# Performance work log

Measured on AMD Instinct MI355X. Metric: run time of the kernel, lower is better.

The kernel has to match this reference:

```python
import jax, jax.numpy as jnp
import numpy as np

N = 20000
E = 320000
F_IN = 256
HID = 32
HEADS = 8
EDGE_DIM = HID // 4  # 8
NEG_SLOPE = 0.2


def _gat_conv(x, src, dst, e_emb, W, att_s, att_d, W_e, att_e, bias, H, C):
    """PyG-style GATConv with edge_dim, add_self_loops=True (fill_value='mean'), concat heads."""
    n = x.shape[0]
    loop = jnp.arange(n, dtype=src.dtype)
    # self-loop edge_attr = scatter-mean of edge_attr by dst (0 for isolated nodes)
    deg = jax.ops.segment_sum(jnp.ones_like(dst, dtype=x.dtype), dst, num_segments=n)
    e_mean = jax.ops.segment_sum(e_emb, dst, num_segments=n) / jnp.maximum(deg, 1.0)[:, None]
    src_a = jnp.concatenate([src, loop])
    dst_a = jnp.concatenate([dst, loop])
    e_all = jnp.concatenate([e_emb, e_mean], axis=0)  # [E+N, edge_dim]

    h = (x @ W).reshape(n, H, C)                      # [N,H,C]
    a_src = jnp.einsum('nhc,hc->nh', h, att_s)        # [N,H]
    a_dst = jnp.einsum('nhc,hc->nh', h, att_d)
    he = (e_all @ W_e).reshape(-1, H, C)              # [E+N,H,C]
    a_edge = jnp.einsum('ehc,hc->eh', he, att_e)      # [E+N,H]

    alpha = jax.nn.leaky_relu(a_src[src_a] + a_dst[dst_a] + a_edge, NEG_SLOPE)
    # segment softmax over destination nodes
    amax = jax.ops.segment_max(alpha, dst_a, num_segments=n)
    alpha = jnp.exp(alpha - amax[dst_a])
    denom = jax.ops.segment_sum(alpha, dst_a, num_segments=n)
    alpha = alpha / (denom[dst_a] + 1e-16)

    msg = h[src_a] * alpha[:, :, None]                # [E+N,H,C]
    out = jax.ops.segment_sum(msg, dst_a, num_segments=n)  # [N,H,C]
    return out.reshape(n, H * C) + bias


def setup_inputs() -> dict:
    key = jax.random.key(0)
    ks = jax.random.split(key, 16)

    def glorot(k, shape):
        fan_in, fan_out = shape[0], shape[-1]
        s = np.sqrt(6.0 / (fan_in + fan_out))
        return jax.random.uniform(k, shape, jnp.float32, -s, s)

    x = jax.random.normal(ks[0], (N, F_IN), jnp.float32)
    edge_index = jax.random.randint(ks[1], (2, E), 0, N, jnp.int32)
    edge_attr = jax.random.uniform(ks[2], (E, 2), jnp.float32)

    # spatial_embed: Linear(2 -> EDGE_DIM)
    Wse = glorot(ks[3], (2, EDGE_DIM))
    bse = jnp.zeros((EDGE_DIM,), jnp.float32)
    # conv1: in=F_IN, heads=HEADS, out=HID, edge_dim=EDGE_DIM
    W1 = glorot(ks[4], (F_IN, HEADS * HID))
    as1 = glorot(ks[5], (HEADS, HID))
    ad1 = glorot(ks[6], (HEADS, HID))
    We1 = glorot(ks[7], (EDGE_DIM, HEADS * HID))
    ae1 = glorot(ks[8], (HEADS, HID))
    b1 = jnp.zeros((HEADS * HID,), jnp.float32)
    # conv2: in=HEADS*HID, heads=1, out=HID
    W2 = glorot(ks[9], (HEADS * HID, HID))
    as2 = glorot(ks[10], (1, HID))
    ad2 = glorot(ks[11], (1, HID))
    We2 = glorot(ks[12], (EDGE_DIM, HID))
    ae2 = glorot(ks[13], (1, HID))
    b2 = jnp.zeros((HID,), jnp.float32)

    return {"x": x, "edge_index": edge_index, "edge_attr": edge_attr,
            "Wse": Wse, "bse": bse,
            "W1": W1, "as1": as1, "ad1": ad1, "We1": We1, "ae1": ae1, "b1": b1,
            "W2": W2, "as2": as2, "ad2": ad2, "We2": We2, "ae2": ae2, "b2": b2}


def reference(x, edge_index, edge_attr, Wse, bse,
              W1, as1, ad1, We1, ae1, b1,
              W2, as2, ad2, We2, ae2, b2):
    src, dst = edge_index[0], edge_index[1]
    e = jax.nn.relu(edge_attr @ Wse + bse)            # [E, EDGE_DIM]
    h = _gat_conv(x, src, dst, e, W1, as1, ad1, We1, ae1, b1, HEADS, HID)
    h = jax.nn.relu(h)                                # dropout inactive (eval)
    out = _gat_conv(h, src, dst, e, W2, as2, ad2, We2, ae2, b2, 1, HID)
    return out
```

## Files before the change

kernel.cpp:

```cpp
#include <hip/hip_runtime.h>
#include <hip/hip_bf16.h>
#include <float.h>


typedef short v8s __attribute__((ext_vector_type(8)));
typedef float v4f __attribute__((ext_vector_type(4)));

__device__ __forceinline__ ushort f2bf(float f) {
  unsigned u = __float_as_uint(f);
  u = (u + 0x7FFF + ((u >> 16) & 1)) >> 16;
  return (ushort)u;
}
__device__ __forceinline__ float bf2f(ushort h) {
  return __uint_as_float(((unsigned)h) << 16);
}
__device__ __forceinline__ unsigned pk2bf(float lo, float hi) {
  return (unsigned)f2bf(lo) | ((unsigned)f2bf(hi) << 16);
}

__global__ __launch_bounds__(256) void k_pre(const int* __restrict__ dst,
                                             const float* __restrict__ W1,
                                             const float* __restrict__ We1,
                                             const float* __restrict__ ae1,
                                             const float* __restrict__ We2,
                                             const float* __restrict__ ae2,
                                             int* __restrict__ deg,
                                             ushort* __restrict__ Bt,
                                             float* __restrict__ M1,
                                             float* __restrict__ m2,
                                             int E, int DB) {
  int b = blockIdx.x;
  if (b < DB) {
    int e = b * 256 + threadIdx.x;
    if (e < E) atomicAdd(&deg[dst[e]], 1);
    return;
  }
  if (b == DB + 64) {
    int t = threadIdx.x;
    if (t < 64) {
      int k = t >> 3, h = t & 7;
      float s = 0.f;
      for (int c = 0; c < 32; c++) s += We1[k * 256 + h * 32 + c] * ae1[h * 32 + c];
      M1[k * 8 + h] = s;
    } else if (t < 72) {
      int k = t - 64;
      float s = 0.f;
      for (int c = 0; c < 32; c++) s += We2[k * 32 + c] * ae2[c];
      m2[k] = s;
    }
    return;
  }
  int b2 = b - DB;
  __shared__ float tile[32][33];
  int bx = b2 & 7, by = b2 >> 3;
  int tx = threadIdx.x & 31, ty = threadIdx.x >> 5;
  for (int r = ty; r < 32; r += 8)
    tile[r][tx] = W1[(size_t)(by * 32 + r) * 256 + bx * 32 + tx];
  __syncthreads();
  for (int r = ty; r < 32; r += 8)
    Bt[(size_t)(bx * 32 + r) * 256 + by * 32 + tx] = f2bf(tile[tx][r]);
}

__global__ __launch_bounds__(1024) void k_scan(const int* __restrict__ deg,
                                               int* __restrict__ row_ptr, int N) {
  __shared__ int part[1024];
  int tid = threadIdx.x;
  int chunk = (N + 1023) / 1024;
  int lo = tid * chunk;
  if (lo > N) lo = N;
  int hi = lo + chunk;
  if (hi > N) hi = N;
  int s = 0;
  for (int i = lo; i < hi; i++) s += deg[i];
  part[tid] = s;
  __syncthreads();
  for (int off = 1; off < 1024; off <<= 1) {
    int v = 0;
    if (tid >= off) v = part[tid - off];
    __syncthreads();
    part[tid] += v;
    __syncthreads();
  }
  int base = part[tid] - s;
  for (int i = lo; i < hi; i++) { row_ptr[i] = base; base += deg[i]; }
  if (tid == 1023) row_ptr[N] = part[1023];
}

__global__ void k_scatter(const int* __restrict__ src, const int* __restrict__ dst,
                          const float* __restrict__ ea,
                          const float* __restrict__ Wse, const float* __restrict__ bse,
                          const float* __restrict__ M1, const float* __restrict__ m2,
                          const int* __restrict__ row_ptr, int* __restrict__ cursor,
                          int* __restrict__ csr_src, float* __restrict__ csr_aed1,
                          float* __restrict__ csr_aed2, int E) {
  __shared__ float sW[16], sb[8], sM[64], sm2[8];
  int t = threadIdx.x;
  if (t < 16) sW[t] = Wse[t];
  if (t < 8) sb[t] = bse[t];
  if (t < 64) sM[t] = M1[t];
  if (t >= 64 && t < 72) sm2[t - 64] = m2[t - 64];
  __syncthreads();
  int i = blockIdx.x * blockDim.x + t;
  if (i >= E) return;
  float2 av = ((const float2*)ea)[i];
  float e8[8];
#pragma unroll
  for (int k = 0; k < 8; k++)
    e8[k] = fmaxf(av.x * sW[k] + av.y * sW[8 + k] + sb[k], 0.f);
  float o[8];
#pragma unroll
  for (int h = 0; h < 8; h++) {
    float s = 0.f;
#pragma unroll
    for (int k = 0; k < 8; k++) s += e8[k] * sM[k * 8 + h];
    o[h] = s;
  }
  float s2 = 0.f;
#pragma unroll
  for (int k = 0; k < 8; k++) s2 += e8[k] * sm2[k];
  int d = dst[i];
  int pos = row_ptr[d] + atomicAdd(&cursor[d], 1);
  csr_src[pos] = src[i];
  *(float4*)(csr_aed1 + (size_t)pos * 8)     = make_float4(o[0], o[1], o[2], o[3]);
  *(float4*)(csr_aed1 + (size_t)pos * 8 + 4) = make_float4(o[4], o[5], o[6], o[7]);
  csr_aed2[pos] = s2;
}

__global__ __launch_bounds__(256) void k_gemm1_mfma(const float* __restrict__ A,
                                                    const ushort* __restrict__ Bt,
                                                    const float* __restrict__ as1,
                                                    const float* __restrict__ ad1,
                                                    ushort* __restrict__ h1b,
                                                    float* __restrict__ asv,
                                                    float* __restrict__ adv, int M) {
  __shared__ ushort sA[64 * 40];
  __shared__ ushort sB[256 * 40];
  __shared__ float sas[256], sad[256];
  int t = threadIdx.x;
  int wave = t >> 6, lane = t & 63;
  int m0 = blockIdx.x * 64;
  int c = lane & 15, kg = lane >> 4;
  sas[t] = as1[t];
  sad[t] = ad1[t];
  v4f acc[4][4];
#pragma unroll
  for (int a = 0; a < 4; a++)
#pragma unroll
    for (int b = 0; b < 4; b++) acc[a][b] = (v4f)(0.f);
  int arow = t >> 2;
  int akoff = (t & 3) * 8;
  bool aval = (m0 + arow) < M;
  const float* aptr = A + (size_t)(m0 + arow) * 256 + akoff;
  const ushort* bptr = Bt + (size_t)t * 256;
  for (int k0 = 0; k0 < 256; k0 += 32) {
    float4 v0 = make_float4(0.f, 0.f, 0.f, 0.f), v1 = v0;
    if (aval) { v0 = *(const float4*)(aptr + k0); v1 = *(const float4*)(aptr + k0 + 4); }
    unsigned* dst32 = (unsigned*)&sA[arow * 40 + akoff];
    dst32[0] = pk2bf(v0.x, v0.y);
    dst32[1] = pk2bf(v0.z, v0.w);
    dst32[2] = pk2bf(v1.x, v1.y);
    dst32[3] = pk2bf(v1.z, v1.w);
    *(v8s*)&sB[t * 40 + 0]  = *(const v8s*)(bptr + k0 + 0);
    *(v8s*)&sB[t * 40 + 8]  = *(const v8s*)(bptr + k0 + 8);
    *(v8s*)&sB[t * 40 + 16] = *(const v8s*)(bptr + k0 + 16);
    *(v8s*)&sB[t * 40 + 24] = *(const v8s*)(bptr + k0 + 24);
    __syncthreads();
    v8s af[4], bfr[4];
#pragma unroll
    for (int mt = 0; mt < 4; mt++) af[mt] = *(v8s*)&sA[(mt * 16 + c) * 40 + kg * 8];
#pragma unroll
    for (int nt = 0; nt < 4; nt++) bfr[nt] = *(v8s*)&sB[(wave * 64 + nt * 16 + c) * 40 + kg * 8];
#pragma unroll
    for (int mt = 0; mt < 4; mt++)
#pragma unroll
      for (int nt = 0; nt < 4; nt++)
        acc[mt][nt] = __builtin_amdgcn_mfma_f32_16x16x32_bf16(af[mt], bfr[nt], acc[mt][nt], 0, 0, 0);
    __syncthreads();
  }
  int colbase = wave * 64;
#pragma unroll
  for (int mt = 0; mt < 4; mt++) {
#pragma unroll
    for (int i = 0; i < 4; i++) {
      int m = m0 + mt * 16 + kg * 4 + i;
      if (m < M) {
#pragma unroll
        for (int nt = 0; nt < 4; nt++)
          h1b[(size_t)m * 256 + colbase + nt * 16 + c] = f2bf(acc[mt][nt][i]);
      }
      float s1a = acc[mt][0][i] * sas[colbase + c]      + acc[mt][1][i] * sas[colbase + 16 + c];
      float s2a = acc[mt][0][i] * sad[colbase + c]      + acc[mt][1][i] * sad[colbase + 16 + c];
      float s1b = acc[mt][2][i] * sas[colbase + 32 + c] + acc[mt][3][i] * sas[colbase + 48 + c];
      float s2b = acc[mt][2][i] * sad[colbase + 32 + c] + acc[mt][3][i] * sad[colbase + 48 + c];
#pragma unroll
      for (int o = 1; o < 16; o <<= 1) {
        s1a += __shfl_xor(s1a, o);
        s2a += __shfl_xor(s2a, o);
        s1b += __shfl_xor(s1b, o);
        s2b += __shfl_xor(s2b, o);
      }
      if (c == 0 && m < M) {
        asv[(size_t)m * 8 + 2 * wave]     = s1a;
        adv[(size_t)m * 8 + 2 * wave]     = s2a;
        asv[(size_t)m * 8 + 2 * wave + 1] = s1b;
        adv[(size_t)m * 8 + 2 * wave + 1] = s2b;
      }
    }
  }
}

__global__ __launch_bounds__(64) void k_conv1(
    const int* __restrict__ row_ptr, const int* __restrict__ csr_src,
    const float* __restrict__ csr_aed1, const float* __restrict__ asv,
    const float* __restrict__ adv, const ushort* __restrict__ h1b,
    const float* __restrict__ b1, ushort* __restrict__ h2b, int N) {
  int n = blockIdx.x;
  int lane = threadIdx.x;
  int h = lane >> 3;
  int sub = lane & 7;
  int hh = lane & 7;
  __shared__ float sw[64 * 8];
  __shared__ int ssrc[64];
  __shared__ float sm[8], sl[8], sadv[8], smean[8];
  int begin = row_ptr[n], end = row_ptr[n + 1];
  int degr = end - begin;
  if (lane < 8) { sm[lane] = -FLT_MAX; sl[lane] = 0.f; sadv[lane] = adv[(size_t)n * 8 + lane]; }
  float aedsum = 0.f;
  float4 acc = make_float4(0.f, 0.f, 0.f, 0.f);
  for (int cs = begin; cs < end; cs += 64) {
    int c = min(64, end - cs);
    __syncthreads();
    if (lane < c) ssrc[lane] = csr_src[cs + lane];
    __syncthreads();
    for (int idx = lane; idx < c * 8; idx += 64) {
      int el = idx >> 3;
      float ae = csr_aed1[(size_t)(cs + el) * 8 + hh];
      aedsum += ae;
      float a = asv[(size_t)ssrc[el] * 8 + hh] + sadv[hh] + ae;
      a = a > 0.f ? a : 0.2f * a;
      sw[idx] = a;
    }
    __syncthreads();
    float mloc = -FLT_MAX;
    for (int el = sub; el < c; el += 8) mloc = fmaxf(mloc, sw[el * 8 + h]);
#pragma unroll
    for (int o = 1; o < 8; o <<= 1) mloc = fmaxf(mloc, __shfl_xor(mloc, o));
    float mold = sm[h];
    float mnew = fmaxf(mold, mloc);
    float scale = __expf(mold - mnew);
    float lloc = 0.f;
    for (int el = sub; el < c; el += 8) {
      float w = __expf(sw[el * 8 + h] - mnew);
      sw[el * 8 + h] = w;
      lloc += w;
    }
#pragma unroll
    for (int o = 1; o < 8; o <<= 1) lloc += __shfl_xor(lloc, o);
    __syncthreads();
    if (sub == 0) { sm[h] = mnew; sl[h] = sl[h] * scale + lloc; }
    acc.x *= scale; acc.y *= scale; acc.z *= scale; acc.w *= scale;
    for (int el = 0; el < c; el++) {
      float w = sw[el * 8 + h];
      ushort4 hv = *(const ushort4*)(h1b + (size_t)ssrc[el] * 256 + lane * 4);
      acc.x += w * bf2f(hv.x);
      acc.y += w * bf2f(hv.y);
      acc.z += w * bf2f(hv.z);
      acc.w += w * bf2f(hv.w);
    }
  }
  aedsum += __shfl_xor(aedsum, 8);
  aedsum += __shfl_xor(aedsum, 16);
  aedsum += __shfl_xor(aedsum, 32);
  float invd = 1.f / (float)(degr > 1 ? degr : 1);
  if (lane < 8) smean[lane] = aedsum * invd;
  __syncthreads();
  float a_self = asv[(size_t)n * 8 + h] + sadv[h] + smean[h];
  a_self = a_self > 0.f ? a_self : 0.2f * a_self;
  float mold = sm[h];
  float mnew = fmaxf(mold, a_self);
  float scale = __expf(mold - mnew);
  float w_self = __expf(a_self - mnew);
  float l_fin = sl[h] * scale + w_self;
  ushort4 hs = *(const ushort4*)(h1b + (size_t)n * 256 + lane * 4);
  acc.x = acc.x * scale + w_self * bf2f(hs.x);
  acc.y = acc.y * scale + w_self * bf2f(hs.y);
  acc.z = acc.z * scale + w_self * bf2f(hs.z);
  acc.w = acc.w * scale + w_self * bf2f(hs.w);
  float inv = 1.f / (l_fin + 1e-16f);
  float4 bv = *(const float4*)(b1 + lane * 4);
  ushort4 o4;
  o4.x = f2bf(fmaxf(acc.x * inv + bv.x, 0.f));
  o4.y = f2bf(fmaxf(acc.y * inv + bv.y, 0.f));
  o4.z = f2bf(fmaxf(acc.z * inv + bv.z, 0.f));
  o4.w = f2bf(fmaxf(acc.w * inv + bv.w, 0.f));
  *(ushort4*)(h2b + (size_t)n * 256 + lane * 4) = o4;
}

__global__ __launch_bounds__(256) void k_gemm2(const ushort* __restrict__ h2b,
                                               const float* __restrict__ W2,
                                               const float* __restrict__ as2,
                                               const float* __restrict__ ad2,
                                               float* __restrict__ g2,
                                               float* __restrict__ asv2,
                                               float* __restrict__ adv2, int N) {
  __shared__ float xs[8 * 256];
  __shared__ float sas[32], sad[32];
  int t = threadIdx.x;
  if (t < 32) { sas[t] = as2[t]; sad[t] = ad2[t]; }
  int n0 = blockIdx.x * 8;
  for (int idx = t; idx < 8 * 256; idx += 256) {
    int node = n0 + (idx >> 8);
    xs[idx] = (node < N) ? bf2f(h2b[(size_t)node * 256 + (idx & 255)]) : 0.f;
  }
  __syncthreads();
  int j = t >> 5, cc = t & 31;
  int node = n0 + j;
  float acc = 0.f;
#pragma unroll 8
  for (int k = 0; k < 256; k++) acc += xs[j * 256 + k] * W2[k * 32 + cc];
  float s1 = acc * sas[cc], s2 = acc * sad[cc];
#pragma unroll
  for (int o = 1; o < 32; o <<= 1) {
    s1 += __shfl_xor(s1, o);
    s2 += __shfl_xor(s2, o);
  }
  if (node < N) {
    g2[(size_t)node * 32 + cc] = acc;
    if (cc == 0) { asv2[node] = s1; adv2[node] = s2; }
  }
}

__global__ __launch_bounds__(64) void k_conv2(
    const int* __restrict__ row_ptr, const int* __restrict__ csr_src,
    const float* __restrict__ csr_aed2, const float* __restrict__ asv2,
    const float* __restrict__ adv2, const float* __restrict__ g2,
    const float* __restrict__ b2, float* __restrict__ out, int N) {
  int n = blockIdx.x;
  int lane = threadIdx.x;
  int sub = lane >> 3, q = lane & 7;
  __shared__ float sw[64];
  __shared__ int ssrc[64];
  int begin = row_ptr[n], end = row_ptr[n + 1];
  int degr = end - begin;
  float advn = adv2[n];
  float m = -FLT_MAX, l = 0.f, aedsum = 0.f;
  float4 acc = make_float4(0.f, 0.f, 0.f, 0.f);
  for (int cs = begin; cs < end; cs += 64) {
    int c = min(64, end - cs);
    __syncthreads();
    float a = -FLT_MAX;
    if (lane < c) {
      int s = csr_src[cs + lane];
      ssrc[lane] = s;
      float ae = csr_aed2[cs + lane];
      aedsum += ae;
      a = asv2[s] + advn + ae;
      a = a > 0.f ? a : 0.2f * a;
    }
    float cm = a;
#pragma unroll
    for (int o = 1; o < 64; o <<= 1) cm = fmaxf(cm, __shfl_xor(cm, o));
    float nm = fmaxf(m, cm);
    float sc = __expf(m - nm);
    float w = (lane < c) ? __expf(a - nm) : 0.f;
    float cl = w;
#pragma unroll
    for (int o = 1; o < 64; o <<= 1) cl += __shfl_xor(cl, o);
    l = l * sc + cl;
    m = nm;
    sw[lane] = w;
    __syncthreads();
    acc.x *= sc; acc.y *= sc; acc.z *= sc; acc.w *= sc;
    for (int el = sub; el < c; el += 8) {
      float w2 = sw[el];
      const float4 gv = *(const float4*)(g2 + (size_t)ssrc[el] * 32 + q * 4);
      acc.x += w2 * gv.x; acc.y += w2 * gv.y; acc.z += w2 * gv.z; acc.w += w2 * gv.w;
    }
  }
#pragma unroll
  for (int o = 1; o < 64; o <<= 1) aedsum += __shfl_xor(aedsum, o);
  float invd = 1.f / (float)(degr > 1 ? degr : 1);
  float a_self = asv2[n] + advn + aedsum * invd;
  a_self = a_self > 0.f ? a_self : 0.2f * a_self;
  float nm = fmaxf(m, a_self);
  float sc = __expf(m - nm);
  float w_self = __expf(a_self - nm);
  l = l * sc + w_self;
  acc.x *= sc; acc.y *= sc; acc.z *= sc; acc.w *= sc;
  if (sub == 0) {
    const float4 gv = *(const float4*)(g2 + (size_t)n * 32 + q * 4);
    acc.x += w_self * gv.x; acc.y += w_self * gv.y;
    acc.z += w_self * gv.z; acc.w += w_self * gv.w;
  }
#pragma unroll
  for (int o = 8; o < 64; o <<= 1) {
    acc.x += __shfl_xor(acc.x, o);
    acc.y += __shfl_xor(acc.y, o);
    acc.z += __shfl_xor(acc.z, o);
    acc.w += __shfl_xor(acc.w, o);
  }
  if (lane < 8) {
    float inv = 1.f / (l + 1e-16f);
    float4 bv = *(const float4*)(b2 + lane * 4);
    float4 o4;
    o4.x = acc.x * inv + bv.x;
    o4.y = acc.y * inv + bv.y;
    o4.z = acc.z * inv + bv.z;
    o4.w = acc.w * inv + bv.w;
    *(float4*)(out + (size_t)n * 32 + lane * 4) = o4;
  }
}

extern "C" void kernel_launch(void* const* d_in, const int* in_sizes, int n_in,
                              void* d_out, int out_size, void* d_ws, size_t ws_size,
                              hipStream_t stream) {
  (void)n_in; (void)out_size; (void)ws_size;
  const float* x   = (const float*)d_in[0];
  const int*   ei  = (const int*)d_in[1];
  const float* ea  = (const float*)d_in[2];
  const float* Wse = (const float*)d_in[3];
  const float* bse = (const float*)d_in[4];
  const float* W1  = (const float*)d_in[5];
  const float* as1 = (const float*)d_in[6];
  const float* ad1 = (const float*)d_in[7];
  const float* We1 = (const float*)d_in[8];
  const float* ae1 = (const float*)d_in[9];
  const float* b1  = (const float*)d_in[10];
  const float* W2  = (const float*)d_in[11];
  const float* as2 = (const float*)d_in[12];
  const float* ad2 = (const float*)d_in[13];
  const float* We2 = (const float*)d_in[14];
  const float* ae2 = (const float*)d_in[15];
  const float* b2  = (const float*)d_in[16];
  const int N = in_sizes[0] / 256;
  const int E = in_sizes[1] / 2;
  const int* src = ei;
  const int* dst = ei + E;

  char* base = (char*)d_ws;
  size_t off = 0;
  auto alloc = [&](size_t bytes) -> char* {
    off = (off + 255) & ~(size_t)255;
    char* p = base + off;
    off += bytes;
    return p;
  };
  int*   deg      = (int*)alloc((size_t)N * 4);
  int*   cursor   = (int*)alloc((size_t)N * 4);
  size_t zero_bytes = (size_t)((char*)(cursor + N) - (char*)deg);
  int* row_ptr    = (int*)alloc((size_t)(N + 1) * 4);
  int* csr_src    = (int*)alloc((size_t)E * 4);
  float* csr_aed1 = (float*)alloc((size_t)E * 8 * 4);
  float* csr_aed2 = (float*)alloc((size_t)E * 4);
  ushort* W1T     = (ushort*)alloc((size_t)256 * 256 * 2);
  ushort* h1b     = (ushort*)alloc((size_t)N * 256 * 2);
  float* asv1     = (float*)alloc((size_t)N * 8 * 4);
  float* adv1     = (float*)alloc((size_t)N * 8 * 4);
  ushort* h2b     = (ushort*)alloc((size_t)N * 256 * 2);
  float* g2       = (float*)alloc((size_t)N * 32 * 4);
  float* asv2     = (float*)alloc((size_t)N * 4);
  float* adv2     = (float*)alloc((size_t)N * 4);
  float* M1       = (float*)alloc(64 * 4);
  float* m2       = (float*)alloc(8 * 4);

  const int DB = (E + 255) / 256;
  hipMemsetAsync(deg, 0, zero_bytes, stream);
  k_pre<<<DB + 65, 256, 0, stream>>>(dst, W1, We1, ae1, We2, ae2, deg, W1T, M1, m2, E, DB);
  k_scan<<<1, 1024, 0, stream>>>(deg, row_ptr, N);
  k_scatter<<<DB, 256, 0, stream>>>(src, dst, ea, Wse, bse, M1, m2, row_ptr, cursor,
                                    csr_src, csr_aed1, csr_aed2, E);
  k_gemm1_mfma<<<(N + 63) / 64, 256, 0, stream>>>(x, W1T, as1, ad1, h1b, asv1, adv1, N);
  k_conv1<<<N, 64, 0, stream>>>(row_ptr, csr_src, csr_aed1, asv1, adv1, h1b, b1, h2b, N);
  k_gemm2<<<(N + 7) / 8, 256, 0, stream>>>(h2b, W2, as2, ad2, g2, asv2, adv2, N);
  k_conv2<<<N, 64, 0, stream>>>(row_ptr, csr_src, csr_aed2, asv2, adv2, g2, b2,
                                (float*)d_out, N);
}
```

Measured before the change: 257.0 us.

## Pack per-edge CSR data into 32-byte records with fp16 edge logits

Replaces the three separate CSR arrays (src index, 8 fp32 edge attention terms, conv2 edge term) with one interleaved 32-byte record per edge, storing the conv1 edge terms as fp16. This cuts the bytes written in the scatter kernel and turns the per-edge reads in both conv kernels into loads from a single cache line. Cursor zeroing moves into the scan kernel so the memset shrinks, and the conv1 aggregation loop gets an unroll-by-2 hint. The fp16 edge logits add a small precision loss, and conv2 now reads strided records instead of a dense array.

```diff
diff --git a/kernel.cpp b/kernel.cpp
--- a/kernel.cpp
+++ b/kernel.cpp
@@ -1,5 +1,6 @@
 #include <hip/hip_runtime.h>
 #include <hip/hip_bf16.h>
+#include <hip/hip_fp16.h>
 #include <float.h>
 
 
@@ -16,6 +17,10 @@
 }
 __device__ __forceinline__ unsigned pk2bf(float lo, float hi) {
   return (unsigned)f2bf(lo) | ((unsigned)f2bf(hi) << 16);
+}
+__device__ __forceinline__ unsigned pk2h(float lo, float hi) {
+  return (unsigned)__half_as_ushort(__float2half(lo)) |
+         ((unsigned)__half_as_ushort(__float2half(hi)) << 16);
 }
 
 __global__ __launch_bounds__(256) void k_pre(const int* __restrict__ dst,
@@ -62,7 +67,8 @@
 }
 
 __global__ __launch_bounds__(1024) void k_scan(const int* __restrict__ deg,
-                                               int* __restrict__ row_ptr, int N) {
+                                               int* __restrict__ row_ptr,
+                                               int* __restrict__ cursor, int N) {
   __shared__ int part[1024];
   int tid = threadIdx.x;
   int chunk = (N + 1023) / 1024;
@@ -71,7 +77,7 @@
   int hi = lo + chunk;
   if (hi > N) hi = N;
   int s = 0;
-  for (int i = lo; i < hi; i++) s += deg[i];
+  for (int i = lo; i < hi; i++) { s += deg[i]; cursor[i] = 0; }
   part[tid] = s;
   __syncthreads();
   for (int off = 1; off < 1024; off <<= 1) {
@@ -91,8 +97,7 @@
                           const float* __restrict__ Wse, const float* __restrict__ bse,
                           const float* __restrict__ M1, const float* __restrict__ m2,
                           const int* __restrict__ row_ptr, int* __restrict__ cursor,
-                          int* __restrict__ csr_src, float* __restrict__ csr_aed1,
-                          float* __restrict__ csr_aed2, int E) {
+                          char* __restrict__ rec, int E) {
   __shared__ float sW[16], sb[8], sM[64], sm2[8];
   int t = threadIdx.x;
   if (t < 16) sW[t] = Wse[t];
@@ -120,10 +125,16 @@
   for (int k = 0; k < 8; k++) s2 += e8[k] * sm2[k];
   int d = dst[i];
   int pos = row_ptr[d] + atomicAdd(&cursor[d], 1);
-  csr_src[pos] = src[i];
-  *(float4*)(csr_aed1 + (size_t)pos * 8)     = make_float4(o[0], o[1], o[2], o[3]);
-  *(float4*)(csr_aed1 + (size_t)pos * 8 + 4) = make_float4(o[4], o[5], o[6], o[7]);
-  csr_aed2[pos] = s2;
+  uint4 w0, w1;
+  w0.x = (unsigned)src[i];
+  w0.y = pk2h(o[0], o[1]);
+  w0.z = pk2h(o[2], o[3]);
+  w0.w = pk2h(o[4], o[5]);
+  w1.x = pk2h(o[6], o[7]);
+  w1.y = __float_as_uint(s2);
+  w1.z = 0; w1.w = 0;
+  *(uint4*)(rec + (size_t)pos * 32)      = w0;
+  *(uint4*)(rec + (size_t)pos * 32 + 16) = w1;
 }
 
 __global__ __launch_bounds__(256) void k_gemm1_mfma(const float* __restrict__ A,
@@ -210,10 +221,10 @@
 }
 
 __global__ __launch_bounds__(64) void k_conv1(
-    const int* __restrict__ row_ptr, const int* __restrict__ csr_src,
-    const float* __restrict__ csr_aed1, const float* __restrict__ asv,
-    const float* __restrict__ adv, const ushort* __restrict__ h1b,
-    const float* __restrict__ b1, ushort* __restrict__ h2b, int N) {
+    const int* __restrict__ row_ptr, const char* __restrict__ rec,
+    const float* __restrict__ asv, const float* __restrict__ adv,
+    const ushort* __restrict__ h1b, const float* __restrict__ b1,
+    ushort* __restrict__ h2b, int N) {
   int n = blockIdx.x;
   int lane = threadIdx.x;
   int h = lane >> 3;
@@ -230,11 +241,11 @@
   for (int cs = begin; cs < end; cs += 64) {
     int c = min(64, end - cs);
     __syncthreads();
-    if (lane < c) ssrc[lane] = csr_src[cs + lane];
+    if (lane < c) ssrc[lane] = *(const int*)(rec + (size_t)(cs + lane) * 32);
     __syncthreads();
     for (int idx = lane; idx < c * 8; idx += 64) {
       int el = idx >> 3;
-      float ae = csr_aed1[(size_t)(cs + el) * 8 + hh];
+      float ae = __half2float(*(const __half*)(rec + (size_t)(cs + el) * 32 + 4 + hh * 2));
       aedsum += ae;
       float a = asv[(size_t)ssrc[el] * 8 + hh] + sadv[hh] + ae;
       a = a > 0.f ? a : 0.2f * a;
@@ -259,6 +270,7 @@
     __syncthreads();
     if (sub == 0) { sm[h] = mnew; sl[h] = sl[h] * scale + lloc; }
     acc.x *= scale; acc.y *= scale; acc.z *= scale; acc.w *= scale;
+#pragma unroll 2
     for (int el = 0; el < c; el++) {
       float w = sw[el * 8 + h];
       ushort4 hv = *(const ushort4*)(h1b + (size_t)ssrc[el] * 256 + lane * 4);
@@ -331,10 +343,10 @@
 }
 
 __global__ __launch_bounds__(64) void k_conv2(
-    const int* __restrict__ row_ptr, const int* __restrict__ csr_src,
-    const float* __restrict__ csr_aed2, const float* __restrict__ asv2,
-    const float* __restrict__ adv2, const float* __restrict__ g2,
-    const float* __restrict__ b2, float* __restrict__ out, int N) {
+    const int* __restrict__ row_ptr, const char* __restrict__ rec,
+    const float* __restrict__ asv2, const float* __restrict__ adv2,
+    const float* __restrict__ g2, const float* __restrict__ b2,
+    float* __restrict__ out, int N) {
   int n = blockIdx.x;
   int lane = threadIdx.x;
   int sub = lane >> 3, q = lane & 7;
@@ -350,9 +362,10 @@
     __syncthreads();
     float a = -FLT_MAX;
     if (lane < c) {
-      int s = csr_src[cs + lane];
+      const char* rp = rec + (size_t)(cs + lane) * 32;
+      int s = *(const int*)rp;
       ssrc[lane] = s;
-      float ae = csr_aed2[cs + lane];
+      float ae = *(const float*)(rp + 20);
       aedsum += ae;
       a = asv2[s] + advn + ae;
       a = a > 0.f ? a : 0.2f * a;
@@ -447,11 +460,8 @@
   };
   int*   deg      = (int*)alloc((size_t)N * 4);
   int*   cursor   = (int*)alloc((size_t)N * 4);
-  size_t zero_bytes = (size_t)((char*)(cursor + N) - (char*)deg);
   int* row_ptr    = (int*)alloc((size_t)(N + 1) * 4);
-  int* csr_src    = (int*)alloc((size_t)E * 4);
-  float* csr_aed1 = (float*)alloc((size_t)E * 8 * 4);
-  float* csr_aed2 = (float*)alloc((size_t)E * 4);
+  char* rec       = alloc((size_t)E * 32);
   ushort* W1T     = (ushort*)alloc((size_t)256 * 256 * 2);
   ushort* h1b     = (ushort*)alloc((size_t)N * 256 * 2);
   float* asv1     = (float*)alloc((size_t)N * 8 * 4);
@@ -464,14 +474,13 @@
   float* m2       = (float*)alloc(8 * 4);
 
   const int DB = (E + 255) / 256;
-  hipMemsetAsync(deg, 0, zero_bytes, stream);
+  hipMemsetAsync(deg, 0, (size_t)N * 4, stream);
   k_pre<<<DB + 65, 256, 0, stream>>>(dst, W1, We1, ae1, We2, ae2, deg, W1T, M1, m2, E, DB);
-  k_scan<<<1, 1024, 0, stream>>>(deg, row_ptr, N);
+  k_scan<<<1, 1024, 0, stream>>>(deg, row_ptr, cursor, N);
   k_scatter<<<DB, 256, 0, stream>>>(src, dst, ea, Wse, bse, M1, m2, row_ptr, cursor,
-                                    csr_src, csr_aed1, csr_aed2, E);
+                                    rec, E);
   k_gemm1_mfma<<<(N + 63) / 64, 256, 0, stream>>>(x, W1T, as1, ad1, h1b, asv1, adv1, N);
-  k_conv1<<<N, 64, 0, stream>>>(row_ptr, csr_src, csr_aed1, asv1, adv1, h1b, b1, h2b, N);
+  k_conv1<<<N, 64, 0, stream>>>(row_ptr, rec, asv1, adv1, h1b, b1, h2b, N);
   k_gemm2<<<(N + 7) / 8, 256, 0, stream>>>(h2b, W2, as2, ad2, g2, asv2, adv2, N);
-  k_conv2<<<N, 64, 0, stream>>>(row_ptr, csr_src, csr_aed2, asv2, adv2, g2, b2,
-                                (float*)d_out, N);
-}
+  k_conv2<<<N, 64, 0, stream>>>(row_ptr, rec, asv2, adv2, g2, b2, (float*)d_out, N);
+}
```

Measured after the change: 256.2 us. No clear change (-0.3%).
